# Kernel optimization log

Hardware: AMD Instinct MI355X
Metric: run time of the kernel (lower is better)

Reference implementation:

```python
import jax, jax.numpy as jnp
import numpy as np

B, SQ, SKV, D, H = 2, 2048, 2048, 1024, 16
DH = D // H


def setup_inputs() -> dict:
    key = jax.random.key(0)
    ks = jax.random.split(key, 4)
    s = 0.02
    return {
        "query_input": jax.random.normal(ks[0], (B, SQ, D), jnp.float32),
        "kv_input": jax.random.normal(ks[1], (B, SKV, D), jnp.float32),
        "Wq": jax.random.normal(ks[2], (D, D), jnp.float32) * s,
        "bq": jnp.zeros((D,), jnp.float32),
        "Wkv": jax.random.normal(ks[3], (D, 2 * D), jnp.float32) * s,
        "bkv": jnp.zeros((2 * D,), jnp.float32),
        "Wo": jax.random.normal(jax.random.fold_in(key, 7), (D, D), jnp.float32) * s,
        "bo": jnp.zeros((D,), jnp.float32),
    }


def reference(query_input, kv_input, Wq, bq, Wkv, bkv, Wo, bo):
    scale = 1.0 / jnp.sqrt(jnp.float32(DH))
    # Projections
    q = query_input @ Wq + bq                      # [B, SQ, D]
    kv = kv_input @ Wkv + bkv                      # [B, SKV, 2D]
    k, v = jnp.split(kv, 2, axis=-1)               # [B, SKV, D] each
    # Split heads: [B, H, S, DH]
    q = q.reshape(B, SQ, H, DH).transpose(0, 2, 1, 3)
    k = k.reshape(B, SKV, H, DH).transpose(0, 2, 1, 3)
    v = v.reshape(B, SKV, H, DH).transpose(0, 2, 1, 3)
    # Scores S = QK^T / sqrt(d_k)
    scores = jnp.einsum("bhqd,bhkd->bhqk", q, k) * scale
    attn = jax.nn.softmax(scores, axis=-1)
    out = jnp.einsum("bhqk,bhkd->bhqd", attn, v)   # [B, H, SQ, DH]
    out = out.transpose(0, 2, 1, 3).reshape(B, SQ, D)
    return out @ Wo + bo
```

## Files before the change

### kernel.cpp

```cpp
#include <hip/hip_runtime.h>

typedef unsigned short u16;
typedef unsigned int u32;
typedef __bf16 bf16x8 __attribute__((ext_vector_type(8)));
typedef __bf16 bf16x2 __attribute__((ext_vector_type(2)));
typedef float f32x4 __attribute__((ext_vector_type(4)));
typedef float f32x16 __attribute__((ext_vector_type(16)));

#define QSCALE 0.18033688011112f

__device__ __forceinline__ u16 f2bf(float f) {
  u32 u = __builtin_bit_cast(u32, f);
  u += 0x7fffu + ((u >> 16) & 1u);
  return (u16)(u >> 16);
}

__device__ __forceinline__ u32 pkbf(float a, float b) {
  bf16x2 t = {(__bf16)a, (__bf16)b};
  return __builtin_bit_cast(u32, t);
}

__device__ __forceinline__ bf16x8 as_bf16x8(uint4 v) {
  return __builtin_bit_cast(bf16x8, v);
}

__device__ __forceinline__ void async16(const void* g, void* l) {
  __builtin_amdgcn_global_load_lds(
      (__attribute__((address_space(1))) void*)(g),
      (__attribute__((address_space(3))) void*)(l), 16, 0, 0);
}

__global__ void prep_kernel(const float* __restrict__ xq, const float* __restrict__ xkv,
                            const float* __restrict__ Wq, const float* __restrict__ Wkv,
                            const float* __restrict__ Wo,
                            u16* __restrict__ Xq16, u16* __restrict__ Xkv16,
                            u16* __restrict__ WqT, u16* __restrict__ WkvT,
                            u16* __restrict__ WoT) {
  const int bid = blockIdx.x, tid = threadIdx.x;
  if (bid < 8192) {
    int i = bid * 256 + tid;
    const float* s; u16* d; int j;
    if (i < 1048576) { s = xq; d = Xq16; j = i; }
    else             { s = xkv; d = Xkv16; j = i - 1048576; }
    float4 v = ((const float4*)s)[j];
    ushort4 o;
    o.x = f2bf(v.x); o.y = f2bf(v.y); o.z = f2bf(v.z); o.w = f2bf(v.w);
    ((ushort4*)d)[j] = o;
    return;
  }
  const int b2 = bid - 8192;
  const int z = b2 >> 11, rem = b2 & 2047;
  const int by = rem >> 6, bx = rem & 63;
  const float* src; u16* dst; int Nd;
  if (z == 0)      { src = Wq;  dst = WqT;  Nd = 1024; }
  else if (z == 1) { src = Wkv; dst = WkvT; Nd = 2048; }
  else             { src = Wo;  dst = WoT;  Nd = 1024; }
  const int n0 = bx * 32, k0 = by * 32;
  if (n0 >= Nd) return;
  __shared__ float tile[32][33];
  const int tx = tid & 31, ty = tid >> 5;
#pragma unroll
  for (int j = 0; j < 4; ++j)
    tile[ty + 8 * j][tx] = src[(size_t)(k0 + ty + 8 * j) * Nd + n0 + tx];
  __syncthreads();
#pragma unroll
  for (int j = 0; j < 4; ++j)
    dst[(size_t)(n0 + ty + 8 * j) * 1024 + k0 + tx] = f2bf(tile[tx][ty + 8 * j]);
}

template <int MI>
static __device__ __forceinline__ void gemm_core(
    const u16* __restrict__ A, const u16* __restrict__ Bt, int m0,
    uint4* sA, uint4* sB, f32x4 (*acc)[4]) {
  const int tid = threadIdx.x;
  const int wv = tid >> 6, lane = tid & 63;
  const int quad = lane >> 4, l16 = lane & 15;
  const int wm = (wv >> 1) * (MI * 16), wn = (wv & 1) * 64;

  const int ib0 = wv * 128 + lane, ib1 = ib0 + 64;
  const int br0 = ib0 >> 2, bc0 = (ib0 & 3) ^ ((br0 >> 1) & 3);
  const int br1 = ib1 >> 2, bc1 = (ib1 & 3) ^ ((br1 >> 1) & 3);
  const u16* gB0 = Bt + (size_t)br0 * 1024 + bc0 * 8;
  const u16* gB1 = Bt + (size_t)br1 * 1024 + bc1 * 8;

  const int ia0 = wv * (MI * 32) + lane;
  const int ar0 = ia0 >> 2, ac0 = (ia0 & 3) ^ ((ar0 >> 1) & 3);
  const u16* gA0 = A + (size_t)(m0 + ar0) * 1024 + ac0 * 8;
  const int ia1 = ia0 + 64;
  const int ar1 = ia1 >> 2, ac1 = (ia1 & 3) ^ ((ar1 >> 1) & 3);
  const u16* gA1 = A + (size_t)(m0 + ar1) * 1024 + ac1 * 8;

  uint4* sAw = sA + wv * (MI * 32);
  uint4* sBw = sB + wv * 128;
  const int ABUF = MI * 128;

  async16(gA0, sAw);
  if (MI == 4) async16(gA1, sAw + 64);
  async16(gB0, sBw);
  async16(gB1, sBw + 64);

  for (int k0 = 0; k0 < 1024; k0 += 32) {
    const int cur = (k0 >> 5) & 1;
    __syncthreads();
    if (k0 < 1024 - 32) {
      const int nx = cur ^ 1;
      async16(gA0 + k0 + 32, sAw + nx * ABUF);
      if (MI == 4) async16(gA1 + k0 + 32, sAw + nx * ABUF + 64);
      async16(gB0 + k0 + 32, sBw + nx * 512);
      async16(gB1 + k0 + 32, sBw + nx * 512 + 64);
    }
    const uint4* A_ = sA + cur * ABUF;
    const uint4* B_ = sB + cur * 512;

    bf16x8 af[MI], bfr[4];
#pragma unroll
    for (int mi = 0; mi < MI; ++mi) {
      int r = wm + mi * 16 + l16;
      af[mi] = as_bf16x8(A_[r * 4 + (quad ^ ((r >> 1) & 3))]);
    }
#pragma unroll
    for (int ni = 0; ni < 4; ++ni) {
      int r = wn + ni * 16 + l16;
      bfr[ni] = as_bf16x8(B_[r * 4 + (quad ^ ((r >> 1) & 3))]);
    }
#pragma unroll
    for (int mi = 0; mi < MI; ++mi)
#pragma unroll
      for (int ni = 0; ni < 4; ++ni)
        acc[mi][ni] = __builtin_amdgcn_mfma_f32_16x16x32_bf16(
            af[mi], bfr[ni], acc[mi][ni], 0, 0, 0);
  }
}

__global__ __launch_bounds__(256, 4) void gemm_qkv(
    const u16* __restrict__ Xq, const u16* __restrict__ Xkv,
    const u16* __restrict__ WqT, const u16* __restrict__ WkvT,
    const float* __restrict__ bq, const float* __restrict__ bkv,
    u16* __restrict__ Qd, u16* __restrict__ Kd, u16* __restrict__ Vd) {
  __shared__ uint4 sA[1024], sB[1024];
  f32x4 acc[4][4] = {};
  const int n0 = blockIdx.x * 128, m0 = blockIdx.y * 128;
  const u16* A = (n0 < 1024) ? Xq : Xkv;
  const u16* Bt = (n0 < 1024) ? (WqT + (size_t)n0 * 1024)
                              : (WkvT + (size_t)(n0 - 1024) * 1024);
  const float* bias = (n0 < 1024) ? (bq + n0) : (bkv + (n0 - 1024));
  gemm_core<4>(A, Bt, m0, sA, sB, acc);

  const int tid = threadIdx.x, wv = tid >> 6, lane = tid & 63;
  const int quad = lane >> 4, l16 = lane & 15;
  const int wm = (wv >> 1) * 64, wn = (wv & 1) * 64;
  const int bb = m0 >> 11;
  const int gmb = m0 + wm + quad * 4;
  const int ssb = (m0 & 2047) + wm + quad * 4;
#pragma unroll
  for (int ni = 0; ni < 4; ++ni) {
    const int gn = n0 + wn + ni * 16 + l16;
    const float bvn = bias[wn + ni * 16 + l16];
    if (gn < 1024) {
      u16* base = Qd + gn;
#pragma unroll
      for (int mi = 0; mi < 4; ++mi)
#pragma unroll
        for (int r = 0; r < 4; ++r)
          base[(size_t)(gmb + mi * 16 + r) * 1024] = f2bf((acc[mi][ni][r] + bvn) * QSCALE);
    } else if (gn < 2048) {
      u16* base = Kd + (gn - 1024);
#pragma unroll
      for (int mi = 0; mi < 4; ++mi)
#pragma unroll
        for (int r = 0; r < 4; ++r)
          base[(size_t)(gmb + mi * 16 + r) * 1024] = f2bf(acc[mi][ni][r] + bvn);
    } else {
      const int col = gn - 2048, hh = col >> 6, dh = col & 63;
      u16* base = Vd + ((size_t)(bb * 16 + hh) * 64 + dh) * 2048 + ssb;
#pragma unroll
      for (int mi = 0; mi < 4; ++mi) {
        ushort4 o;
        o.x = f2bf(acc[mi][ni][0] + bvn);
        o.y = f2bf(acc[mi][ni][1] + bvn);
        o.z = f2bf(acc[mi][ni][2] + bvn);
        o.w = f2bf(acc[mi][ni][3] + bvn);
        *(ushort4*)(base + mi * 16) = o;
      }
    }
  }
}

__global__ __launch_bounds__(512, 4) void flash_attn(
    const u16* __restrict__ Q, const u16* __restrict__ K,
    const u16* __restrict__ V, u16* __restrict__ O) {
  __shared__ uint4 sbuf[4096];
  __shared__ float sLB[128];
  __shared__ float sLA[128];

  const int tid = threadIdx.x;
  const int wv = tid >> 6, lane = tid & 63;
  const int grp = wv >> 2, wq = wv & 3;
  const int c = lane & 31, hh = lane >> 5;
  const int hb = blockIdx.x & 31;
  const int q0 = (blockIdx.x >> 5) * 128;
  const int h = hb & 15, bz = hb >> 4;

  const u16* Qb = Q + ((size_t)(bz * 2048 + q0 + wq * 32)) * 1024 + h * 64;
  const u16* Kb = K + ((size_t)(bz * 2048 + grp * 64)) * 1024 + h * 64;
  const u16* Vb = V + ((size_t)(bz * 16 + h)) * 64 * 2048 + grp * 64;

  uint4* sKg = sbuf + grp * 1024;
  uint4* sVg = sbuf + 2048 + grp * 1024;

  const int i0 = wq * 128 + lane, i1 = i0 + 64;
  const int r0 = i0 >> 3, r1 = i1 >> 3;
  const int ck0 = (i0 & 7) ^ (r0 & 7), ck1 = (i1 & 7) ^ (r1 & 7);
  const u16* gK0 = Kb + (size_t)r0 * 1024 + ck0 * 8;
  const u16* gK1 = Kb + (size_t)r1 * 1024 + ck1 * 8;
  const u16* gV0 = Vb + (size_t)r0 * 2048 + ck0 * 8;
  const u16* gV1 = Vb + (size_t)r1 * 2048 + ck1 * 8;
  const int wo = wq * 128;

  bf16x8 qf[4];
  {
    const u16* qr = Qb + (size_t)c * 1024 + hh * 8;
#pragma unroll
    for (int s = 0; s < 4; ++s)
      qf[s] = as_bf16x8(*(const uint4*)(qr + 16 * s));
  }

  f32x16 oacc[2] = {};
  float lp = 0.f;

  async16(gK0, sKg + wo);
  async16(gK1, sKg + wo + 64);
  async16(gV0, sVg + wo);
  async16(gV1, sVg + wo + 64);

  for (int t = 0; t < 16; ++t) {
    const int cur = t & 1;
    __syncthreads();
    if (t < 15) {
      const size_t ko = (size_t)(t + 1) * 128 * 1024;
      const int vo = (t + 1) * 128;
      async16(gK0 + ko, sKg + (cur ^ 1) * 512 + wo);
      async16(gK1 + ko, sKg + (cur ^ 1) * 512 + wo + 64);
      async16(gV0 + vo, sVg + (cur ^ 1) * 512 + wo);
      async16(gV1 + vo, sVg + (cur ^ 1) * 512 + wo + 64);
    }
    const uint4* K_ = sKg + cur * 512;
    const uint4* V_ = sVg + cur * 512;

    bf16x8 kf[2][4];
#pragma unroll
    for (int b = 0; b < 2; ++b) {
      const int row = 32 * b + c, sw = row & 7;
#pragma unroll
      for (int s = 0; s < 4; ++s)
        kf[b][s] = as_bf16x8(K_[row * 8 + ((2 * s + hh) ^ sw)]);
    }

    bf16x8 pa[4];
#pragma unroll
    for (int b = 0; b < 2; ++b) {
      f32x16 sAcc = {};
      __builtin_amdgcn_s_setprio(1);
#pragma unroll
      for (int s = 0; s < 4; ++s)
        sAcc = __builtin_amdgcn_mfma_f32_32x32x16_bf16(kf[b][s], qf[s], sAcc, 0, 0, 0);
      __builtin_amdgcn_s_setprio(0);
      float e[16];
#pragma unroll
      for (int r = 0; r < 16; ++r) e[r] = __builtin_amdgcn_exp2f(sAcc[r]);
      float t0 = (e[0] + e[1]) + (e[2] + e[3]);
      float t1 = (e[4] + e[5]) + (e[6] + e[7]);
      float t2 = (e[8] + e[9]) + (e[10] + e[11]);
      float t3 = (e[12] + e[13]) + (e[14] + e[15]);
      lp += (t0 + t1) + (t2 + t3);
      u32 wA0 = pkbf(e[0], e[1]),   wA1 = pkbf(e[2], e[3]);
      u32 wB0 = pkbf(e[4], e[5]),   wB1 = pkbf(e[6], e[7]);
      u32 wC0 = pkbf(e[8], e[9]),   wC1 = pkbf(e[10], e[11]);
      u32 wD0 = pkbf(e[12], e[13]), wD1 = pkbf(e[14], e[15]);
      asm("v_permlane32_swap_b32 %0, %1" : "+v"(wA0), "+v"(wB0));
      asm("v_permlane32_swap_b32 %0, %1" : "+v"(wA1), "+v"(wB1));
      asm("v_permlane32_swap_b32 %0, %1" : "+v"(wC0), "+v"(wD0));
      asm("v_permlane32_swap_b32 %0, %1" : "+v"(wC1), "+v"(wD1));
      uint4 f0 = {wA0, wA1, wB0, wB1};
      uint4 f1 = {wC0, wC1, wD0, wD1};
      pa[2 * b]     = as_bf16x8(f0);
      pa[2 * b + 1] = as_bf16x8(f1);
    }

    bf16x8 vf[2][4];
#pragma unroll
    for (int nb = 0; nb < 2; ++nb) {
      const int row = 32 * nb + c, sw = row & 7;
#pragma unroll
      for (int ks = 0; ks < 4; ++ks)
        vf[nb][ks] = as_bf16x8(V_[row * 8 + ((2 * ks + hh) ^ sw)]);
    }

    __builtin_amdgcn_s_setprio(1);
#pragma unroll
    for (int nb = 0; nb < 2; ++nb)
#pragma unroll
      for (int ks = 0; ks < 4; ++ks)
        oacc[nb] = __builtin_amdgcn_mfma_f32_32x32x16_bf16(
            pa[ks], vf[nb][ks], oacc[nb], 0, 0, 0);
    __builtin_amdgcn_s_setprio(0);
  }

  float rtot;
  {
    u32 a = __builtin_bit_cast(u32, lp);
    u32 b = a;
    asm("v_permlane32_swap_b32 %0, %1" : "+v"(a), "+v"(b));
    rtot = __builtin_bit_cast(float, a) + __builtin_bit_cast(float, b);
  }
  if (grp) sLB[wq * 32 + c] = rtot;

  __syncthreads();
  float* scr = (float*)sbuf;

  if (grp) {
#pragma unroll
    for (int nb = 0; nb < 2; ++nb) {
      float* dst = scr + (wq * 2 + nb) * 1024;
#pragma unroll
      for (int r = 0; r < 16; ++r)
        dst[r * 64 + lane] = oacc[nb][r];
    }
  }
  __syncthreads();
  if (!grp) {
#pragma unroll
    for (int nb = 0; nb < 2; ++nb) {
      const float* sp = scr + (wq * 2 + nb) * 1024;
#pragma unroll
      for (int r = 0; r < 16; ++r)
        oacc[nb][r] += sp[r * 64 + lane];
    }
    float tot = rtot + sLB[wq * 32 + c];
    sLA[wq * 32 + c] = 1.0f / tot;

    u16* Ob = O + ((size_t)(bz * 2048 + q0 + wq * 32)) * 1024 + h * 64;
#pragma unroll
    for (int nb = 0; nb < 2; ++nb)
#pragma unroll
      for (int r = 0; r < 16; ++r) {
        const int qr = (r & 3) + 8 * (r >> 2) + 4 * hh;
        float rl = sLA[wq * 32 + qr];
        Ob[(size_t)qr * 1024 + nb * 32 + c] = f2bf(oacc[nb][r] * rl);
      }
  }
}

__global__ __launch_bounds__(256, 4) void gemm_out(
    const u16* __restrict__ A, const u16* __restrict__ Bt,
    const float* __restrict__ bias, float* __restrict__ C) {
  __shared__ uint4 sA[512], sB[1024];
  f32x4 acc[2][4] = {};
  const int n0 = blockIdx.x * 128, m0 = blockIdx.y * 64;
  gemm_core<2>(A, Bt + (size_t)n0 * 1024, m0, sA, sB, acc);

  const int tid = threadIdx.x, wv = tid >> 6, lane = tid & 63;
  const int quad = lane >> 4, l16 = lane & 15;
  const int wm = (wv >> 1) * 32, wn = (wv & 1) * 64;
  float bv[4];
#pragma unroll
  for (int ni = 0; ni < 4; ++ni) bv[ni] = bias[n0 + wn + ni * 16 + l16];
#pragma unroll
  for (int mi = 0; mi < 2; ++mi)
#pragma unroll
    for (int ni = 0; ni < 4; ++ni)
#pragma unroll
      for (int r = 0; r < 4; ++r) {
        int gm = m0 + wm + mi * 16 + quad * 4 + r;
        int gn = n0 + wn + ni * 16 + l16;
        C[(size_t)gm * 1024 + gn] = acc[mi][ni][r] + bv[ni];
      }
}

extern "C" void kernel_launch(void* const* d_in, const int* in_sizes, int n_in,
                              void* d_out, int out_size, void* d_ws, size_t ws_size,
                              hipStream_t stream) {
  const float* xq  = (const float*)d_in[0];
  const float* xkv = (const float*)d_in[1];
  const float* Wq  = (const float*)d_in[2];
  const float* bq  = (const float*)d_in[3];
  const float* Wkv = (const float*)d_in[4];
  const float* bkv = (const float*)d_in[5];
  const float* Wo  = (const float*)d_in[6];
  const float* bo  = (const float*)d_in[7];
  float* out = (float*)d_out;

  char* p = (char*)d_ws;
  u16* Xq16  = (u16*)p; p += (size_t)8 << 20;
  u16* Xkv16 = (u16*)p; p += (size_t)8 << 20;
  u16* WqT   = (u16*)p; p += (size_t)2 << 20;
  u16* WkvT  = (u16*)p; p += (size_t)4 << 20;
  u16* WoT   = (u16*)p; p += (size_t)2 << 20;
  u16* Q16   = (u16*)p; p += (size_t)8 << 20;
  u16* K16   = (u16*)p; p += (size_t)8 << 20;
  u16* Vt16  = (u16*)p; p += (size_t)8 << 20;
  u16* O16   = (u16*)p; p += (size_t)8 << 20;

  prep_kernel<<<14336, 256, 0, stream>>>(xq, xkv, Wq, Wkv, Wo,
                                         Xq16, Xkv16, WqT, WkvT, WoT);
  gemm_qkv<<<dim3(24, 32), 256, 0, stream>>>(Xq16, Xkv16, WqT, WkvT, bq, bkv,
                                             Q16, K16, Vt16);
  flash_attn<<<512, 512, 0, stream>>>(Q16, K16, Vt16, O16);
  gemm_out<<<dim3(8, 64), 256, 0, stream>>>(O16, WoT, bo, out);
}
```

Before: 201.7 us.

## Triple-buffer GEMM K-loop with explicit vmcnt waits and prefetch depth two

The shared GEMM core moves from a double-buffered K loop with __syncthreads to a three-stage ring buffer. Loads run two K-steps ahead, and each step waits with an explicit s_waitcnt vmcnt count before a raw s_barrier, so global-to-LDS latency overlaps more with MFMA work. The cost is 1.5x the LDS per block and a lower occupancy hint for the QKV GEMM (launch bounds 4 to 3). The hand-written vmcnt counts must match the number of outstanding async loads per thread.

```diff
diff --git a/kernel.cpp b/kernel.cpp
--- a/kernel.cpp
+++ b/kernel.cpp
@@ -98,19 +98,31 @@
   if (MI == 4) async16(gA1, sAw + 64);
   async16(gB0, sBw);
   async16(gB1, sBw + 64);
-
-  for (int k0 = 0; k0 < 1024; k0 += 32) {
-    const int cur = (k0 >> 5) & 1;
-    __syncthreads();
-    if (k0 < 1024 - 32) {
-      const int nx = cur ^ 1;
-      async16(gA0 + k0 + 32, sAw + nx * ABUF);
-      if (MI == 4) async16(gA1 + k0 + 32, sAw + nx * ABUF + 64);
-      async16(gB0 + k0 + 32, sBw + nx * 512);
-      async16(gB1 + k0 + 32, sBw + nx * 512 + 64);
-    }
-    const uint4* A_ = sA + cur * ABUF;
-    const uint4* B_ = sB + cur * 512;
+  async16(gA0 + 32, sAw + ABUF);
+  if (MI == 4) async16(gA1 + 32, sAw + ABUF + 64);
+  async16(gB0 + 32, sBw + 512);
+  async16(gB1 + 32, sBw + 512 + 64);
+
+  for (int k = 0; k < 32; ++k) {
+    if (k < 31) {
+      if (MI == 4) asm volatile("s_waitcnt vmcnt(4)" ::: "memory");
+      else         asm volatile("s_waitcnt vmcnt(3)" ::: "memory");
+    } else {
+      asm volatile("s_waitcnt vmcnt(0)" ::: "memory");
+    }
+    __builtin_amdgcn_s_barrier();
+    asm volatile("" ::: "memory");
+
+    if (k + 2 < 32) {
+      const int nb = (k + 2) % 3;
+      const int ko = (k + 2) * 32;
+      async16(gA0 + ko, sAw + nb * ABUF);
+      if (MI == 4) async16(gA1 + ko, sAw + nb * ABUF + 64);
+      async16(gB0 + ko, sBw + nb * 512);
+      async16(gB1 + ko, sBw + nb * 512 + 64);
+    }
+    const uint4* A_ = sA + (k % 3) * ABUF;
+    const uint4* B_ = sB + (k % 3) * 512;
 
     bf16x8 af[MI], bfr[4];
 #pragma unroll
@@ -132,12 +144,12 @@
   }
 }
 
-__global__ __launch_bounds__(256, 4) void gemm_qkv(
+__global__ __launch_bounds__(256, 3) void gemm_qkv(
     const u16* __restrict__ Xq, const u16* __restrict__ Xkv,
     const u16* __restrict__ WqT, const u16* __restrict__ WkvT,
     const float* __restrict__ bq, const float* __restrict__ bkv,
     u16* __restrict__ Qd, u16* __restrict__ Kd, u16* __restrict__ Vd) {
-  __shared__ uint4 sA[1024], sB[1024];
+  __shared__ uint4 sA[1536], sB[1536];
   f32x4 acc[4][4] = {};
   const int n0 = blockIdx.x * 128, m0 = blockIdx.y * 128;
   const u16* A = (n0 < 1024) ? Xq : Xkv;
@@ -354,7 +366,7 @@
 __global__ __launch_bounds__(256, 4) void gemm_out(
     const u16* __restrict__ A, const u16* __restrict__ Bt,
     const float* __restrict__ bias, float* __restrict__ C) {
-  __shared__ uint4 sA[512], sB[1024];
+  __shared__ uint4 sA[768], sB[1536];
   f32x4 acc[2][4] = {};
   const int n0 = blockIdx.x * 128, m0 = blockIdx.y * 64;
   gemm_core<2>(A, Bt + (size_t)n0 * 1024, m0, sA, sB, acc);
```

New measurement: 199.1 us. No clear change (-1.3%).
